# Kernel optimization log

Measured on AMD Instinct MI355X. Metric: run time of the kernel, lower is better.

The kernel has to match this reference:

```python
import jax, jax.numpy as jnp
import numpy as np
import math

B, CIN, COUT, H, W, K, SDIM = 8, 512, 512, 64, 64, 3, 512
EPS = 1e-8
NEG_SLOPE = 0.2
SCALE = math.sqrt(2.0)


def setup_inputs() -> dict:
    key = jax.random.key(0)
    ks = jax.random.split(key, 7)
    x = jax.random.normal(ks[0], (B, CIN, H, W), jnp.float32)
    style = jax.random.normal(ks[1], (B, SDIM), jnp.float32)
    noise = jax.random.normal(ks[2], (B, 1, H, W), jnp.float32)
    # kernel stored as (kh, kw, Cin, Cout) like keras Conv2D
    fan_in = K * K * CIN
    kernel = jax.random.normal(ks[3], (K, K, CIN, COUT), jnp.float32) / math.sqrt(fan_in)
    style_scale = jax.random.normal(ks[4], (SDIM, COUT), jnp.float32) * 0.02
    bias = jax.random.normal(ks[5], (COUT,), jnp.float32) * 0.01
    noise_weight = jax.random.normal(ks[6], (1,), jnp.float32) * 0.1
    return {"x": x, "style": style, "noise": noise, "kernel": kernel,
            "style_scale": style_scale, "bias": bias, "noise_weight": noise_weight}


def _styled_conv(x, style, noise, kernel, style_scale, bias, noise_weight):
    b = x.shape[0]
    # --- modulation ---
    s = style @ style_scale                              # [B, Cout]
    w = kernel[None] * (s[:, None, None, None, :] + 1.0)  # [B, kh, kw, Cin, Cout]
    # --- demodulation ---
    d = jax.lax.rsqrt(jnp.sum(jnp.square(w), axis=(1, 2, 3)) + EPS)  # [B, Cout]
    w = w * d[:, None, None, None, :]
    # --- per-sample conv via batch-as-groups trick ---
    # weights -> OIHW with O = B*Cout, groups = B
    w_oihw = jnp.transpose(w, (0, 4, 3, 1, 2)).reshape(b * COUT, CIN, K, K)
    x_g = x.reshape(1, b * CIN, H, W)
    out = jax.lax.conv_general_dilated(
        x_g, w_oihw, window_strides=(1, 1), padding="SAME",
        feature_group_count=b,
        dimension_numbers=("NCHW", "OIHW", "NCHW"))
    out = out.reshape(b, COUT, H, W)
    # --- noise injection ---
    out = out + noise_weight[0] * noise                  # noise broadcasts over channels
    # --- fused bias + leaky relu * sqrt(2) ---
    out = jax.nn.leaky_relu(out + bias[None, :, None, None], NEG_SLOPE) * SCALE
    return out


def reference(x, style, noise, kernel, style_scale, bias, noise_weight):
    return _styled_conv(x, style, noise, kernel, style_scale, bias, noise_weight)
```

## Files before the change

### kernel.cpp

```cpp
#include <hip/hip_runtime.h>

#define B_     8
#define CIN_   512
#define COUT_  512
#define HW_    64
#define SDIM_  512
#define NPIX   4096
#define KTOT   4608
#define PADW   66

typedef __attribute__((ext_vector_type(4))) float f32x4;
typedef __attribute__((ext_vector_type(8))) short bf16x8;
typedef __attribute__((ext_vector_type(8))) unsigned short u16x8;

__device__ __forceinline__ float bf2f(unsigned short b) {
    unsigned int u = ((unsigned int)b) << 16;
    return __builtin_bit_cast(float, u);
}
__device__ __forceinline__ unsigned short f2bf(float f) {
    unsigned int u = __builtin_bit_cast(unsigned int, f);
    return (unsigned short)((u + 0x7fffu + ((u >> 16) & 1u)) >> 16);
}
__device__ __forceinline__ float ldin(const void* p, size_t i, int isbf) {
    return isbf ? bf2f(((const unsigned short*)p)[i]) : ((const float*)p)[i];
}

#define GLD16(g, l) __builtin_amdgcn_global_load_lds( \
    (__attribute__((address_space(1))) void*)(g),     \
    (__attribute__((address_space(3))) void*)(l), 16, 0, 0)

__global__ void detect_dtype(const unsigned int* __restrict__ style_u32,
                             int* __restrict__ flag) {
    int t = threadIdx.x;
    unsigned int w = style_u32[t * 4];
    int e = (w >> 7) & 0xFF;
    int isbf = (e >= 110 && e <= 140) ? 1 : 0;
    __shared__ int cnt;
    if (t == 0) cnt = 0;
    __syncthreads();
    atomicAdd(&cnt, isbf);
    __syncthreads();
    if (t == 0) *flag = (cnt >= 128) ? 1 : 0;
}

__global__ void halo_zero(unsigned int* __restrict__ xtp2u) {
    int idx = blockIdx.x;
    int b = blockIdx.y;
    int y, x;
    if (idx < 66)       { y = 0;  x = idx; }
    else if (idx < 132) { y = 65; x = idx - 66; }
    else if (idx < 196) { x = 0;  y = idx - 131; }
    else                { x = 65; y = idx - 195; }
    int t = threadIdx.x;
    int cit = t >> 5, j = t & 31;
    size_t u32i = ((((size_t)(b * 8 + cit) * 66 + y) * 66 + x) << 5) + j;
    xtp2u[u32i] = 0;
}

__global__ void wt_transpose(const void* __restrict__ kin,
                             unsigned short* __restrict__ wt,
                             const int* __restrict__ flag) {
    __shared__ __align__(16) unsigned short tile[64][72];
    int isbf = *flag;
    int t = threadIdx.x;
    int co0 = blockIdx.x * 64;
    int k0  = blockIdx.y * 64;
    int r = t >> 2, c16 = (t & 3) << 4;
    if (isbf) {
        const unsigned short* src = (const unsigned short*)kin + (size_t)(k0 + r) * COUT_ + co0 + c16;
        *(u16x8*)&tile[r][c16]     = *(const u16x8*)src;
        *(u16x8*)&tile[r][c16 + 8] = *(const u16x8*)(src + 8);
    } else {
        const float* src = (const float*)kin + (size_t)(k0 + r) * COUT_ + co0 + c16;
#pragma unroll
        for (int q = 0; q < 4; ++q) {
            f32x4 v = *(const f32x4*)(src + q * 4);
#pragma unroll
            for (int j = 0; j < 4; ++j) tile[r][c16 + q * 4 + j] = f2bf(v[j]);
        }
    }
    __syncthreads();
    int c = t >> 2, r16 = (t & 3) << 4;
    u16x8 w0, w1;
#pragma unroll
    for (int j = 0; j < 8; ++j) { w0[j] = tile[r16 + j][c]; w1[j] = tile[r16 + 8 + j][c]; }
    unsigned short* dst = wt + (size_t)(co0 + c) * KTOT + k0 + r16;
    *(u16x8*)dst       = w0;
    *(u16x8*)(dst + 8) = w1;
}

__global__ void xpose(const void* __restrict__ x,
                      unsigned short* __restrict__ xtp2,
                      const int* __restrict__ flag) {
    __shared__ __align__(16) unsigned short tile[64][72];
    int isbf = *flag;
    int t = threadIdx.x;
    int cit = blockIdx.x;
    int y   = blockIdx.y;
    int b   = blockIdx.z;
    int ci_l = t >> 2, xo = (t & 3) << 4;
    size_t srcoff = (((size_t)(b * CIN_ + cit * 64 + ci_l)) * HW_ + y) * HW_ + xo;
    if (isbf) {
        const unsigned short* src = (const unsigned short*)x + srcoff;
        *(u16x8*)&tile[ci_l][xo]     = *(const u16x8*)src;
        *(u16x8*)&tile[ci_l][xo + 8] = *(const u16x8*)(src + 8);
    } else {
        const float* src = (const float*)x + srcoff;
#pragma unroll
        for (int q = 0; q < 4; ++q) {
            f32x4 v = *(const f32x4*)(src + q * 4);
#pragma unroll
            for (int j = 0; j < 4; ++j) tile[ci_l][xo + q * 4 + j] = f2bf(v[j]);
        }
    }
    __syncthreads();
    int xl = t >> 2, cio = (t & 3) << 4;
    u16x8 w0, w1;
#pragma unroll
    for (int j = 0; j < 8; ++j) { w0[j] = tile[cio + j][xl]; w1[j] = tile[cio + 8 + j][xl]; }
    unsigned short* dst =
        xtp2 + ((((size_t)(b * 8 + cit) * 66 + (y + 1)) * 66 + (xl + 1)) << 6) + cio;
    *(u16x8*)dst       = w0;
    *(u16x8*)(dst + 8) = w1;
}

__global__ void mod_kernel(const void* __restrict__ style,
                           const void* __restrict__ sscale,
                           const unsigned short* __restrict__ wt,
                           float* __restrict__ mmod,
                           const int* __restrict__ flag) {
    int isbf = *flag;
    int co = blockIdx.x, t = threadIdx.x;
    int lane = t & 63, wid = t >> 6;
    float k2 = 0.f;
    const unsigned short* wr = wt + (size_t)co * KTOT;
    for (int k = t; k < KTOT; k += 256) { float v = bf2f(wr[k]); k2 += v * v; }
    float sb[B_];
#pragma unroll
    for (int b = 0; b < B_; ++b) sb[b] = 0.f;
    for (int sd = t; sd < SDIM_; sd += 256) {
        float ss = ldin(sscale, (size_t)sd * COUT_ + co, isbf);
#pragma unroll
        for (int b = 0; b < B_; ++b) sb[b] += ldin(style, b * SDIM_ + sd, isbf) * ss;
    }
    __shared__ float red[4][9];
    float vals[9];
    vals[0] = k2;
#pragma unroll
    for (int b = 0; b < B_; ++b) vals[1 + b] = sb[b];
#pragma unroll
    for (int q = 0; q < 9; ++q) {
        float v = vals[q];
        for (int off = 32; off; off >>= 1) v += __shfl_down(v, off);
        if (lane == 0) red[wid][q] = v;
    }
    __syncthreads();
    if (t < B_) {
        int b = t;
        float k2t = red[0][0] + red[1][0] + red[2][0] + red[3][0];
        float s   = red[0][1 + b] + red[1][1 + b] + red[2][1 + b] + red[3][1 + b];
        float sp1 = s + 1.f;
        mmod[b * COUT_ + co] = sp1 * rsqrtf(sp1 * sp1 * k2t + 1e-8f);
    }
}

__global__ __launch_bounds__(512, 2) void conv_gemm(
    const unsigned short* __restrict__ wt,
    const unsigned short* __restrict__ xtp2,
    const float* __restrict__ mmod,
    const void* __restrict__ noise,
    const void* __restrict__ bias,
    const void* __restrict__ nwp,
    void* __restrict__ out,
    const int* __restrict__ flag) {
    __shared__ __align__(1024) unsigned short Asm[2][256 * 64];
    __shared__ __align__(1024) unsigned short Win[6 * 72 * 64];
    int isbf = *flag;
    int tid = threadIdx.x;
    int lane = tid & 63, wid = tid >> 6;
    int lr = lane & 15, hi = lane >> 4;
    int wm = wid >> 2, wn = wid & 3;

    int bid = blockIdx.x;
    int swz = (bid & 7) * 32 + (bid >> 3);
    int gy = swz >> 7;
    int nb = swz & 127;
    int b  = nb >> 4;
    int nt = nb & 15;
    int pl0 = nt << 8;
    int h0  = pl0 >> 6;
    int co0 = gy << 8;

    f32x4 acc[8][4];
#pragma unroll
    for (int i = 0; i < 8; ++i)
#pragma unroll
        for (int j = 0; j < 4; ++j) acc[i][j] = (f32x4){0.f, 0.f, 0.f, 0.f};

    int rsub = lane >> 3;
    int ce_src = ((lane & 7) ^ rsub) << 3;
    int swzr = (lane & 7) << 3;
    int wsrc = (rsub << 6) + (((lane & 7) ^ (rsub & 7)) << 3);
    int l7 = lane & 7;
    int px[4];
#pragma unroll
    for (int ni = 0; ni < 4; ++ni) px[ni] = ((ni << 4) + lr) << 6;

    auto stageA = [&](int koff, int pp, int q) {
        const unsigned short* srcA =
            wt + (size_t)(co0 + (q << 6) + (wid << 3) + rsub) * KTOT + koff + ce_src;
        GLD16(srcA, (char*)&Asm[pp][0] + (q << 13) + (wid << 10));
    };
    auto stage_win = [&](int cit) {
        size_t base = ((size_t)(b * 8 + cit) * 66 + h0) * (66 * 64);
        for (int idx = wid; idx < 54; idx += 8) {
            int r = idx / 9, g = idx - r * 9;
            const unsigned short* src = xtp2 + base + (size_t)r * (66 * 64) + (g << 9) + wsrc;
            GLD16(src, (char*)Win + r * 9216 + (g << 10));
        }
    };

    stage_win(0);
#pragma unroll
    for (int q = 0; q < 4; ++q) stageA(0, 0, q);
    asm volatile("s_waitcnt vmcnt(0)" ::: "memory");
    __builtin_amdgcn_s_barrier();
    asm volatile("" ::: "memory");

    int t = 0;
    for (int cit = 0; cit < 8; ++cit) {
        if (cit > 0) {
            stage_win(cit);
            asm volatile("s_waitcnt vmcnt(0)" ::: "memory");
            __builtin_amdgcn_s_barrier();
            asm volatile("" ::: "memory");
        }
        for (int khw = 0; khw < 9; ++khw, ++t) {
            int p = t & 1, pn = p ^ 1;
            const unsigned short* As = &Asm[p][0];
            int kh = (khw >= 6) ? 2 : ((khw >= 3) ? 1 : 0);
            int kw = khw - kh * 3;
            int BD = (((wn + kh) * 72) + kw) << 6;
            int xv = ((l7 + kw) & 7) << 3;

            if (t < 71) {
                int khw1 = (khw == 8) ? 0 : khw + 1;
                int cit1 = (khw == 8) ? cit + 1 : cit;
                int koff1 = khw1 * 512 + (cit1 << 6);
#pragma unroll
                for (int q = 0; q < 4; ++q) stageA(koff1, pn, q);
            }

            bf16x8 a0[4], bk0[4];
            int kc0 = (hi << 3), kc1 = 32 + (hi << 3);
#pragma unroll
            for (int i = 0; i < 4; ++i)
                a0[i] = *(const bf16x8*)&As[(((wm << 7) + (i << 4) + lr) << 6) + (kc0 ^ swzr)];
#pragma unroll
            for (int ni = 0; ni < 4; ++ni)
                bk0[ni] = *(const bf16x8*)&Win[BD + px[ni] + (kc0 ^ xv)];
            __builtin_amdgcn_s_setprio(1);
#pragma unroll
            for (int mf = 0; mf < 4; ++mf)
#pragma unroll
                for (int nf = 0; nf < 4; ++nf)
                    acc[mf][nf] = __builtin_amdgcn_mfma_f32_16x16x32_bf16(a0[mf], bk0[nf], acc[mf][nf], 0, 0, 0);
            __builtin_amdgcn_s_setprio(0);

            bf16x8 a1[4];
#pragma unroll
            for (int i = 0; i < 4; ++i)
                a1[i] = *(const bf16x8*)&As[(((wm << 7) + ((i + 4) << 4) + lr) << 6) + (kc0 ^ swzr)];
            __builtin_amdgcn_s_setprio(1);
#pragma unroll
            for (int mf = 0; mf < 4; ++mf)
#pragma unroll
                for (int nf = 0; nf < 4; ++nf)
                    acc[mf + 4][nf] = __builtin_amdgcn_mfma_f32_16x16x32_bf16(a1[mf], bk0[nf], acc[mf + 4][nf], 0, 0, 0);
            __builtin_amdgcn_s_setprio(0);

            bf16x8 a2[4], bk1[4];
#pragma unroll
            for (int i = 0; i < 4; ++i)
                a2[i] = *(const bf16x8*)&As[(((wm << 7) + (i << 4) + lr) << 6) + (kc1 ^ swzr)];
#pragma unroll
            for (int ni = 0; ni < 4; ++ni)
                bk1[ni] = *(const bf16x8*)&Win[BD + px[ni] + (kc1 ^ xv)];
            __builtin_amdgcn_s_setprio(1);
#pragma unroll
            for (int mf = 0; mf < 4; ++mf)
#pragma unroll
                for (int nf = 0; nf < 4; ++nf)
                    acc[mf][nf] = __builtin_amdgcn_mfma_f32_16x16x32_bf16(a2[mf], bk1[nf], acc[mf][nf], 0, 0, 0);
            __builtin_amdgcn_s_setprio(0);

            bf16x8 a3[4];
#pragma unroll
            for (int i = 0; i < 4; ++i)
                a3[i] = *(const bf16x8*)&As[(((wm << 7) + ((i + 4) << 4) + lr) << 6) + (kc1 ^ swzr)];
            __builtin_amdgcn_s_setprio(1);
#pragma unroll
            for (int mf = 0; mf < 4; ++mf)
#pragma unroll
                for (int nf = 0; nf < 4; ++nf)
                    acc[mf + 4][nf] = __builtin_amdgcn_mfma_f32_16x16x32_bf16(a3[mf], bk1[nf], acc[mf + 4][nf], 0, 0, 0);
            __builtin_amdgcn_s_setprio(0);

            asm volatile("s_waitcnt lgkmcnt(0)" ::: "memory");
            if (t < 71) asm volatile("s_waitcnt vmcnt(0)" ::: "memory");
            __builtin_amdgcn_s_barrier();
            asm volatile("" ::: "memory");
        }
    }

    float nw = ldin(nwp, 0, isbf);
    unsigned short* out16 = (unsigned short*)out;
    float* outf = (float*)out;
#pragma unroll
    for (int mf = 0; mf < 8; ++mf) {
        int cobase = co0 + (wm << 7) + (mf << 4) + (hi << 2);
        f32x4 mv = *(const f32x4*)&mmod[b * COUT_ + cobase];
        float bb[4];
#pragma unroll
        for (int r = 0; r < 4; ++r) bb[r] = ldin(bias, cobase + r, isbf);
#pragma unroll
        for (int nf = 0; nf < 4; ++nf) {
            int pix = pl0 + (wn << 6) + (nf << 4) + lr;
            float nv = nw * ldin(noise, b * NPIX + pix, isbf);
#pragma unroll
            for (int r = 0; r < 4; ++r) {
                float v = acc[mf][nf][r] * mv[r] + nv + bb[r];
                v = (v < 0.f ? v * 0.2f : v) * 1.41421356237f;
                size_t oidx = ((size_t)(b * COUT_ + cobase + r)) * NPIX + pix;
                if (isbf) out16[oidx] = f2bf(v);
                else      outf[oidx]  = v;
            }
        }
    }
}

extern "C" void kernel_launch(void* const* d_in, const int* in_sizes, int n_in,
                              void* d_out, int out_size, void* d_ws, size_t ws_size,
                              hipStream_t stream) {
    const void* x      = d_in[0];
    const void* style  = d_in[1];
    const void* noise  = d_in[2];
    const void* kin    = d_in[3];
    const void* sscale = d_in[4];
    const void* bias   = d_in[5];
    const void* nwp    = d_in[6];

    char* ws = (char*)d_ws;
    int* flag = (int*)ws;
    const size_t xtp_off   = 256;
    const size_t xtp_bytes = (size_t)B_ * 8 * 66 * 66 * 64 * 2;
    const size_t pad       = 4096;
    const size_t wt_bytes  = (size_t)COUT_ * KTOT * 2;
    unsigned short* xtp2 = (unsigned short*)(ws + xtp_off);
    unsigned short* wtr  = (unsigned short*)(ws + xtp_off + xtp_bytes + pad);
    float* mmod          = (float*)(ws + xtp_off + xtp_bytes + pad + wt_bytes);

    detect_dtype<<<1, 256, 0, stream>>>((const unsigned int*)style, flag);
    halo_zero<<<dim3(260, 8), 256, 0, stream>>>((unsigned int*)xtp2);
    wt_transpose<<<dim3(8, 72), 256, 0, stream>>>(kin, wtr, flag);
    xpose<<<dim3(8, 64, 8), 256, 0, stream>>>(x, xtp2, flag);
    mod_kernel<<<512, 256, 0, stream>>>(style, sscale, wtr, mmod, flag);
    conv_gemm<<<256, 512, 0, stream>>>(wtr, xtp2, mmod, noise, bias, nwp, d_out, flag);
}
```

Measured before the change: 185.8 us.

## Load weight fragments directly from global and double-buffer the input window

New measurement: 320.6 us. 72.5% more time.

```diff
diff --git a/kernel.cpp b/kernel.cpp
--- a/kernel.cpp
+++ b/kernel.cpp
@@ -173,8 +173,7 @@
     const void* __restrict__ nwp,
     void* __restrict__ out,
     const int* __restrict__ flag) {
-    __shared__ __align__(1024) unsigned short Asm[2][256 * 64];
-    __shared__ __align__(1024) unsigned short Win[6 * 72 * 64];
+    __shared__ __align__(1024) unsigned short Win[2][6 * 72 * 64];
     int isbf = *flag;
     int tid = threadIdx.x;
     int lane = tid & 63, wid = tid >> 6;
@@ -198,119 +197,65 @@
         for (int j = 0; j < 4; ++j) acc[i][j] = (f32x4){0.f, 0.f, 0.f, 0.f};
 
     int rsub = lane >> 3;
-    int ce_src = ((lane & 7) ^ rsub) << 3;
-    int swzr = (lane & 7) << 3;
     int wsrc = (rsub << 6) + (((lane & 7) ^ (rsub & 7)) << 3);
     int l7 = lane & 7;
     int px[4];
 #pragma unroll
     for (int ni = 0; ni < 4; ++ni) px[ni] = ((ni << 4) + lr) << 6;
 
-    auto stageA = [&](int koff, int pp, int q) {
-        const unsigned short* srcA =
-            wt + (size_t)(co0 + (q << 6) + (wid << 3) + rsub) * KTOT + koff + ce_src;
-        GLD16(srcA, (char*)&Asm[pp][0] + (q << 13) + (wid << 10));
-    };
-    auto stage_win = [&](int cit) {
+    const unsigned short* wa = wt + (size_t)(co0 + (wm << 7) + lr) * KTOT + (hi << 3);
+
+    auto stage_win = [&](int cit, int wb) {
         size_t base = ((size_t)(b * 8 + cit) * 66 + h0) * (66 * 64);
         for (int idx = wid; idx < 54; idx += 8) {
             int r = idx / 9, g = idx - r * 9;
             const unsigned short* src = xtp2 + base + (size_t)r * (66 * 64) + (g << 9) + wsrc;
-            GLD16(src, (char*)Win + r * 9216 + (g << 10));
+            GLD16(src, (char*)&Win[wb][0] + r * 9216 + (g << 10));
         }
     };
 
-    stage_win(0);
-#pragma unroll
-    for (int q = 0; q < 4; ++q) stageA(0, 0, q);
+    stage_win(0, 0);
     asm volatile("s_waitcnt vmcnt(0)" ::: "memory");
     __builtin_amdgcn_s_barrier();
     asm volatile("" ::: "memory");
 
-    int t = 0;
     for (int cit = 0; cit < 8; ++cit) {
-        if (cit > 0) {
-            stage_win(cit);
-            asm volatile("s_waitcnt vmcnt(0)" ::: "memory");
-            __builtin_amdgcn_s_barrier();
-            asm volatile("" ::: "memory");
-        }
-        for (int khw = 0; khw < 9; ++khw, ++t) {
-            int p = t & 1, pn = p ^ 1;
-            const unsigned short* As = &Asm[p][0];
+        int wb = cit & 1;
+        const unsigned short* W = &Win[wb][0];
+        if (cit < 7) stage_win(cit + 1, wb ^ 1);
+
+        for (int khw = 0; khw < 9; ++khw) {
             int kh = (khw >= 6) ? 2 : ((khw >= 3) ? 1 : 0);
             int kw = khw - kh * 3;
             int BD = (((wn + kh) * 72) + kw) << 6;
             int xv = ((l7 + kw) & 7) << 3;
-
-            if (t < 71) {
-                int khw1 = (khw == 8) ? 0 : khw + 1;
-                int cit1 = (khw == 8) ? cit + 1 : cit;
-                int koff1 = khw1 * 512 + (cit1 << 6);
-#pragma unroll
-                for (int q = 0; q < 4; ++q) stageA(koff1, pn, q);
+            const unsigned short* wa_t = wa + khw * 512 + (cit << 6);
+
+#pragma unroll
+            for (int kk = 0; kk < 2; ++kk) {
+                bf16x8 a[8], bk[4];
+                int kc = (kk << 5) + (hi << 3);
+#pragma unroll
+                for (int mf = 0; mf < 8; ++mf)
+                    a[mf] = *(const bf16x8*)(wa_t + (size_t)(mf << 4) * KTOT + (kk << 5));
+#pragma unroll
+                for (int ni = 0; ni < 4; ++ni)
+                    bk[ni] = *(const bf16x8*)&W[BD + px[ni] + (kc ^ xv)];
+                __builtin_amdgcn_s_setprio(1);
+#pragma unroll
+                for (int mf = 0; mf < 8; ++mf)
+#pragma unroll
+                    for (int nf = 0; nf < 4; ++nf)
+                        acc[mf][nf] = __builtin_amdgcn_mfma_f32_16x16x32_bf16(
+                            a[mf], bk[nf], acc[mf][nf], 0, 0, 0);
+                __builtin_amdgcn_s_setprio(0);
             }
-
-            bf16x8 a0[4], bk0[4];
-            int kc0 = (hi << 3), kc1 = 32 + (hi << 3);
-#pragma unroll
-            for (int i = 0; i < 4; ++i)
-                a0[i] = *(const bf16x8*)&As[(((wm << 7) + (i << 4) + lr) << 6) + (kc0 ^ swzr)];
-#pragma unroll
-            for (int ni = 0; ni < 4; ++ni)
-                bk0[ni] = *(const bf16x8*)&Win[BD + px[ni] + (kc0 ^ xv)];
-            __builtin_amdgcn_s_setprio(1);
-#pragma unroll
-            for (int mf = 0; mf < 4; ++mf)
-#pragma unroll
-                for (int nf = 0; nf < 4; ++nf)
-                    acc[mf][nf] = __builtin_amdgcn_mfma_f32_16x16x32_bf16(a0[mf], bk0[nf], acc[mf][nf], 0, 0, 0);
-            __builtin_amdgcn_s_setprio(0);
-
-            bf16x8 a1[4];
-#pragma unroll
-            for (int i = 0; i < 4; ++i)
-                a1[i] = *(const bf16x8*)&As[(((wm << 7) + ((i + 4) << 4) + lr) << 6) + (kc0 ^ swzr)];
-            __builtin_amdgcn_s_setprio(1);
-#pragma unroll
-            for (int mf = 0; mf < 4; ++mf)
-#pragma unroll
-                for (int nf = 0; nf < 4; ++nf)
-                    acc[mf + 4][nf] = __builtin_amdgcn_mfma_f32_16x16x32_bf16(a1[mf], bk0[nf], acc[mf + 4][nf], 0, 0, 0);
-            __builtin_amdgcn_s_setprio(0);
-
-            bf16x8 a2[4], bk1[4];
-#pragma unroll
-            for (int i = 0; i < 4; ++i)
-                a2[i] = *(const bf16x8*)&As[(((wm << 7) + (i << 4) + lr) << 6) + (kc1 ^ swzr)];
-#pragma unroll
-            for (int ni = 0; ni < 4; ++ni)
-                bk1[ni] = *(const bf16x8*)&Win[BD + px[ni] + (kc1 ^ xv)];
-            __builtin_amdgcn_s_setprio(1);
-#pragma unroll
-            for (int mf = 0; mf < 4; ++mf)
-#pragma unroll
-                for (int nf = 0; nf < 4; ++nf)
-                    acc[mf][nf] = __builtin_amdgcn_mfma_f32_16x16x32_bf16(a2[mf], bk1[nf], acc[mf][nf], 0, 0, 0);
-            __builtin_amdgcn_s_setprio(0);
-
-            bf16x8 a3[4];
-#pragma unroll
-            for (int i = 0; i < 4; ++i)
-                a3[i] = *(const bf16x8*)&As[(((wm << 7) + ((i + 4) << 4) + lr) << 6) + (kc1 ^ swzr)];
-            __builtin_amdgcn_s_setprio(1);
-#pragma unroll
-            for (int mf = 0; mf < 4; ++mf)
-#pragma unroll
-                for (int nf = 0; nf < 4; ++nf)
-                    acc[mf + 4][nf] = __builtin_amdgcn_mfma_f32_16x16x32_bf16(a3[mf], bk1[nf], acc[mf + 4][nf], 0, 0, 0);
-            __builtin_amdgcn_s_setprio(0);
-
-            asm volatile("s_waitcnt lgkmcnt(0)" ::: "memory");
-            if (t < 71) asm volatile("s_waitcnt vmcnt(0)" ::: "memory");
-            __builtin_amdgcn_s_barrier();
-            asm volatile("" ::: "memory");
-        }
+        }
+
+        asm volatile("s_waitcnt lgkmcnt(0)" ::: "memory");
+        asm volatile("s_waitcnt vmcnt(0)" ::: "memory");
+        __builtin_amdgcn_s_barrier();
+        asm volatile("" ::: "memory");
     }
 
     float nw = ldin(nwp, 0, isbf);
```
